# Performance work log

Measured on AMD Instinct MI355X. Metric: run time of the kernel, lower is better.

## Reference

```python
import jax, jax.numpy as jnp
import numpy as np

B, K, T, C, F = 2048, 32, 365, 4, 128  # batch, prototypes, steps, bands, feature_size


def conv1d(x, w, b, pad):
    # x: (B, Cin, T), w: (Cout, Cin, Kw)
    y = jax.lax.conv_general_dilated(x, w, (1,), [(pad, pad)],
                                     dimension_numbers=('NCH', 'OIH', 'NCH'))
    return y + b[None, :, None]


def bn_relu(x, gamma, beta):
    # training-mode BatchNorm1d over (batch, time) per channel
    mu = x.mean((0, 2), keepdims=True)
    var = x.var((0, 2), keepdims=True)
    xn = (x - mu) * jax.lax.rsqrt(var + 1e-5)
    return jax.nn.relu(xn * gamma[None, :, None] + beta[None, :, None])


def encoder(x, w1, b1, g1, be1, w2, b2, g2, be2, w3, b3, g3, be3, fc_w, fc_b):
    # FCNBaseline: 3 conv blocks + global average pool + linear
    h = x.transpose(0, 2, 1)                    # (B, C, T)
    h = bn_relu(conv1d(h, w1, b1, 4), g1, be1)  # (B, 128, T+1)
    h = bn_relu(conv1d(h, w2, b2, 2), g2, be2)  # (B, 256, *)
    h = bn_relu(conv1d(h, w3, b3, 1), g3, be3)  # (B, 128, *)
    return h.mean(-1) @ fc_w.T + fc_b           # (B, F)


def setup_inputs() -> dict:
    key = jax.random.key(0)
    ks = jax.random.split(key, 12)
    input_seq = jax.random.normal(ks[0], (B, T, C), jnp.float32)
    label = jax.random.randint(ks[1], (B,), 0, 9)
    mask = (jax.random.uniform(ks[2], (B, T)) > 0.2).astype(jnp.float32)
    prototypes = jax.random.normal(ks[3], (K, T, C), jnp.float32)
    w1 = jax.random.normal(ks[4], (128, C, 8)) * 0.05
    b1 = jnp.zeros((128,)); g1 = jnp.ones((128,)); be1 = jnp.zeros((128,))
    w2 = jax.random.normal(ks[5], (256, 128, 5)) * 0.05
    b2 = jnp.zeros((256,)); g2 = jnp.ones((256,)); be2 = jnp.zeros((256,))
    w3 = jax.random.normal(ks[6], (128, 256, 3)) * 0.05
    b3 = jnp.zeros((128,)); g3 = jnp.ones((128,)); be3 = jnp.zeros((128,))
    fc_w = jax.random.normal(ks[7], (F, 128)) * 0.05
    fc_b = jnp.zeros((F,))
    off_w = jax.random.normal(ks[8], (K * C, F)) * 0.05
    off_b = jnp.zeros((K * C,))
    return dict(input_seq=input_seq, label=label, mask=mask, prototypes=prototypes,
                w1=w1, b1=b1, g1=g1, be1=be1, w2=w2, b2=b2, g2=g2, be2=be2,
                w3=w3, b3=b3, g3=g3, be3=be3, fc_w=fc_w, fc_b=fc_b,
                off_w=off_w, off_b=off_b)


def reference(input_seq, label, mask, prototypes, w1, b1, g1, be1, w2, b2, g2, be2,
              w3, b3, g3, be3, fc_w, fc_b, off_w, off_b):
    # trans_activ=False (TPS warp disabled), offset_activ=True, unsupervised path
    feat = encoder(input_seq, w1, b1, g1, be1, w2, b2, g2, be2, w3, b3, g3, be3, fc_w, fc_b)
    offset = jnp.tanh(feat @ off_w.T + off_b).reshape(-1, K, 1, C)  # (B,K,1,C)
    protos = prototypes[None] + offset                              # (B,K,T,C)
    diff = input_seq[:, None] - protos                              # (B,K,T,C)
    # masked squared-distance reduce: mask (B,T) broadcasts over (K,C)
    distances = jnp.einsum('bktc,bt->bk', diff * diff, mask)        # (B,K)
    indices = jnp.argmin(distances, axis=1)                         # (B,)
    output_seq = jnp.take_along_axis(protos, indices[:, None, None, None], axis=1)[:, 0]
    return output_seq
```

## Files before the change

### kernel.cpp

```cpp
#include <hip/hip_runtime.h>
#include <hip/hip_bf16.h>

#define BB 2048
#define TIN 365
#define TO 366
#define C1 128
#define C2 256
#define C3 128
#define FF 128

typedef __attribute__((ext_vector_type(4))) float f32x4v;
typedef __attribute__((ext_vector_type(8))) short bf16x8;

__device__ inline unsigned short f2bf(float v) {
  unsigned u = __float_as_uint(v);
  unsigned r = (u + 0x7FFF + ((u >> 16) & 1)) >> 16;
  return (unsigned short)r;
}
__device__ inline float bf2f(unsigned short b) {
  return __uint_as_float(((unsigned)b) << 16);
}

__global__ void wtrans_kernel(const float* __restrict__ wsrc, float* __restrict__ wdst,
                              int Cout, int Cin, int Kw) {
  int n = Cout * Cin * Kw;
  for (int idx = blockIdx.x * 256 + threadIdx.x; idx < n; idx += gridDim.x * 256) {
    int o = idx % Cout;
    int rest = idx / Cout;
    int k = rest % Kw;
    int i = rest / Kw;
    wdst[idx] = wsrc[(o * Cin + i) * Kw + k];
  }
}

__global__ void wprep2_kernel(const float* __restrict__ w2,
                              short* __restrict__ wh, short* __restrict__ wl) {
  int n = 256 * 128 * 5;
  for (int idx = blockIdx.x * 256 + threadIdx.x; idx < n; idx += gridDim.x * 256) {
    int k = idx % 5;
    int rest = idx / 5;
    int i = rest % 128;
    int o = rest / 128;
    float v = w2[idx];
    unsigned short hb = f2bf(v);
    unsigned short lb = f2bf(v - bf2f(hb));
    size_t dst = ((((size_t)k * 4 + (i >> 5)) * 16 + (o >> 4)) * 64 +
                  ((i >> 3) & 3) * 16 + (o & 15)) * 8 + (i & 7);
    wh[dst] = (short)hb;
    wl[dst] = (short)lb;
  }
}
__global__ void wprep3_kernel(const float* __restrict__ w3,
                              short* __restrict__ wh, short* __restrict__ wl) {
  int n = 128 * 256 * 3;
  for (int idx = blockIdx.x * 256 + threadIdx.x; idx < n; idx += gridDim.x * 256) {
    int k = idx % 3;
    int rest = idx / 3;
    int i = rest % 256;
    int o = rest / 256;
    float v = w3[idx];
    unsigned short hb = f2bf(v);
    unsigned short lb = f2bf(v - bf2f(hb));
    size_t dst = ((((size_t)k * 8 + (i >> 5)) * 8 + (o >> 4)) * 64 +
                  ((i >> 3) & 3) * 16 + (o & 15)) * 8 + (i & 7);
    wh[dst] = (short)hb;
    wl[dst] = (short)lb;
  }
}

__global__ void bnparam_kernel(const double* __restrict__ sums,
                               const float* __restrict__ gamma,
                               const float* __restrict__ beta, int Cch,
                               float* __restrict__ scale, float* __restrict__ shift) {
  int i = threadIdx.x;
  if (i < Cch) {
    const double N = (double)BB * (double)TO;
    double mean = sums[i] / N;
    double var = sums[Cch + i] / N - mean * mean;
    double sc = (double)gamma[i] / sqrt(var + 1e-5);
    scale[i] = (float)sc;
    shift[i] = (float)((double)beta[i] - mean * sc);
  }
}

__global__ __launch_bounds__(256) void conv1_stats_kernel(
    const float* __restrict__ x, const float* __restrict__ w1,
    const float* __restrict__ b1, double* __restrict__ sums) {
  __shared__ float4 xs[374];
  __shared__ float ws1[4096];
  int tid = threadIdx.x;
  for (int i = tid; i < 4096; i += 256) ws1[i] = w1[i];
  __syncthreads();
  const int o = tid >> 1, half = tid & 1;
  float wr[32];
#pragma unroll
  for (int i = 0; i < 32; ++i) wr[i] = ws1[o * 32 + i];
  const float bo = b1[o];
  float s1 = 0.f, s2 = 0.f;
  for (int b = blockIdx.x * 8; b < blockIdx.x * 8 + 8; ++b) {
    __syncthreads();
    for (int u = tid; u < 374; u += 256) {
      int t_in = u - 4;
      float4 v = make_float4(0.f, 0.f, 0.f, 0.f);
      if (t_in >= 0 && t_in < TIN) v = *(const float4*)(x + ((size_t)b * TIN + t_in) * 4);
      xs[u] = v;
    }
    __syncthreads();
    for (int t = half * 183; t < half * 183 + 183; ++t) {
      float acc = bo;
#pragma unroll
      for (int k = 0; k < 8; ++k) {
        float4 xv = xs[t + k];
        acc = fmaf(wr[k], xv.x, acc);
        acc = fmaf(wr[8 + k], xv.y, acc);
        acc = fmaf(wr[16 + k], xv.z, acc);
        acc = fmaf(wr[24 + k], xv.w, acc);
      }
      s1 += acc; s2 += acc * acc;
    }
  }
  s1 += __shfl_xor(s1, 1);
  s2 += __shfl_xor(s2, 1);
  if (half == 0) {
    atomicAdd(&sums[o], (double)s1);
    atomicAdd(&sums[C1 + o], (double)s2);
  }
}

template <bool STORE>
__global__ __launch_bounds__(256) void conv2_mfma_kernel(
    const float* __restrict__ x, const float* __restrict__ w1g,
    const float* __restrict__ b1, const float* __restrict__ scale1,
    const float* __restrict__ shift1, const short* __restrict__ w2ph,
    const short* __restrict__ w2pl, const float* __restrict__ b2,
    float* __restrict__ p2, float* __restrict__ h2g) {
  __shared__ float ws1[4096];
  __shared__ float4 xwin[76];
  __shared__ __align__(16) short h1h[68 * 72];
  __shared__ __align__(16) short h1l[68 * 72];
  __shared__ float sstat[512];
  const int tid = threadIdx.x;
  const int tt = blockIdx.x, b = blockIdx.y;
  const int tbase = tt * 64;
  const int slice = (b * 6 + tt) & 63;
  const int w = tid >> 6, lane = tid & 63;
  const int q = lane >> 4, l15 = lane & 15;

  for (int i = tid; i < 4096; i += 256) ws1[i] = w1g[i];
  for (int u = tid; u < 76; u += 256) {
    int tx = tbase - 6 + u;
    float4 v = make_float4(0.f, 0.f, 0.f, 0.f);
    if (tx >= 0 && tx < TIN) v = *(const float4*)(x + ((size_t)b * TIN + tx) * 4);
    xwin[u] = v;
  }
  float b2r[4][4];
#pragma unroll
  for (int om = 0; om < 4; ++om)
#pragma unroll
    for (int r = 0; r < 4; ++r) b2r[om][r] = b2[64 * w + om * 16 + q * 4 + r];

  f32x4v acc[4][4];
#pragma unroll
  for (int om = 0; om < 4; ++om)
#pragma unroll
    for (int nt = 0; nt < 4; ++nt) acc[om][nt] = (f32x4v){0.f, 0.f, 0.f, 0.f};

  const int chl = tid >> 2, qt = tid & 3;
  for (int ic2 = 0; ic2 < 2; ++ic2) {
    __syncthreads();
    {
      int ch = ic2 * 64 + chl;
      float sc = scale1[ch], sh = shift1[ch], bo = b1[ch];
      const float* wr = &ws1[ch * 32];
      for (int j = 0; j < 17; ++j) {
        int u = qt * 17 + j;
        int t = tbase - 2 + u;
        float a = bo;
#pragma unroll
        for (int kk = 0; kk < 8; ++kk) {
          float4 xv = xwin[u + kk];
          a = fmaf(wr[kk], xv.x, a);
          a = fmaf(wr[8 + kk], xv.y, a);
          a = fmaf(wr[16 + kk], xv.z, a);
          a = fmaf(wr[24 + kk], xv.w, a);
        }
        float v = (t >= 0 && t < TO) ? fmaxf(fmaf(sc, a, sh), 0.f) : 0.f;
        unsigned short hb = f2bf(v);
        h1h[u * 72 + chl] = (short)hb;
        h1l[u * 72 + chl] = (short)f2bf(v - bf2f(hb));
      }
    }
    __syncthreads();
    for (int k = 0; k < 5; ++k) {
      for (int ic = 0; ic < 2; ++ic) {
        int icg = ic2 * 2 + ic;
        bf16x8 ah[4], al[4];
#pragma unroll
        for (int om = 0; om < 4; ++om) {
          int og = 4 * w + om;
          size_t base = ((((size_t)k * 4 + icg) * 16 + og) * 64 + lane) * 8;
          ah[om] = *(const bf16x8*)(w2ph + base);
          al[om] = *(const bf16x8*)(w2pl + base);
        }
        int ioff = ic * 32 + q * 8;
#pragma unroll
        for (int nt = 0; nt < 4; ++nt) {
          int u = nt * 16 + l15 + k;
          bf16x8 bh = *(const bf16x8*)&h1h[u * 72 + ioff];
          bf16x8 bl = *(const bf16x8*)&h1l[u * 72 + ioff];
#pragma unroll
          for (int om = 0; om < 4; ++om) {
            acc[om][nt] = __builtin_amdgcn_mfma_f32_16x16x32_bf16(ah[om], bh, acc[om][nt], 0, 0, 0);
            acc[om][nt] = __builtin_amdgcn_mfma_f32_16x16x32_bf16(ah[om], bl, acc[om][nt], 0, 0, 0);
            acc[om][nt] = __builtin_amdgcn_mfma_f32_16x16x32_bf16(al[om], bh, acc[om][nt], 0, 0, 0);
          }
        }
      }
    }
  }
  float ts1[16], ts2[16];
#pragma unroll
  for (int i = 0; i < 16; ++i) { ts1[i] = 0.f; ts2[i] = 0.f; }
#pragma unroll
  for (int om = 0; om < 4; ++om)
#pragma unroll
    for (int nt = 0; nt < 4; ++nt) {
      int t = tbase + nt * 16 + l15;
      if (t < TO) {
#pragma unroll
        for (int r = 0; r < 4; ++r) {
          float v = acc[om][nt][r] + b2r[om][r];
          ts1[om * 4 + r] += v;
          ts2[om * 4 + r] += v * v;
          if (STORE) {
            int o = 64 * w + om * 16 + q * 4 + r;
            h2g[((size_t)b * 256 + o) * 368 + t] = v;
          }
        }
      }
    }
#pragma unroll
  for (int i = 0; i < 16; ++i) {
#pragma unroll
    for (int d = 1; d < 16; d <<= 1) {
      ts1[i] += __shfl_xor(ts1[i], d);
      ts2[i] += __shfl_xor(ts2[i], d);
    }
  }
  if (l15 == 0) {
#pragma unroll
    for (int om = 0; om < 4; ++om)
#pragma unroll
      for (int r = 0; r < 4; ++r) {
        int o = 64 * w + om * 16 + q * 4 + r;
        sstat[o] = ts1[om * 4 + r];
        sstat[256 + o] = ts2[om * 4 + r];
      }
  }
  __syncthreads();
  atomicAdd(&p2[(size_t)tid * 64 + slice], sstat[tid]);
  atomicAdd(&p2[((size_t)tid + 256) * 64 + slice], sstat[tid + 256]);
}

template <int EPI>
__global__ __launch_bounds__(256) void conv3_pass_kernel(
    const float* __restrict__ h2g, const float* __restrict__ scale2,
    const float* __restrict__ shift2, const short* __restrict__ w3ph,
    const short* __restrict__ w3pl, const float* __restrict__ b3,
    const float* __restrict__ scale3, const float* __restrict__ shift3,
    float* __restrict__ p3, float* __restrict__ pooled) {
  __shared__ __align__(16) short h2sh[66 * 264];
  __shared__ __align__(16) short h2sl[66 * 264];
  __shared__ float sstat[256];
  const int tid = threadIdx.x;
  const int tt = blockIdx.x, b = blockIdx.y;
  const int tbase = tt * 64;
  const int slice = (b * 6 + tt) & 63;
  const int w = tid >> 6, lane = tid & 63;
  const int q = lane >> 4, l15 = lane & 15;

  float b3r[2][4], sc3r[2][4], sh3r[2][4];
#pragma unroll
  for (int om = 0; om < 2; ++om)
#pragma unroll
    for (int r = 0; r < 4; ++r) {
      int o = 32 * w + om * 16 + q * 4 + r;
      b3r[om][r] = b3[o];
      if (EPI == 1) { sc3r[om][r] = scale3[o]; sh3r[om][r] = shift3[o]; }
    }

  for (int cc = 0; cc < 64; ++cc) {
    int ch = w * 64 + cc;
    float sc = scale2[ch], sh = shift2[ch];
    const float* src = h2g + ((size_t)b * 256 + ch) * 368;
    int t2 = tbase - 1 + lane;
    float v = 0.f;
    if (t2 >= 0 && t2 < TO) v = fmaxf(fmaf(sc, src[t2], sh), 0.f);
    unsigned short hb = f2bf(v);
    h2sh[lane * 264 + ch] = (short)hb;
    h2sl[lane * 264 + ch] = (short)f2bf(v - bf2f(hb));
    if (lane < 2) {
      int u2 = 64 + lane;
      int t2b = tbase - 1 + u2;
      float vb = 0.f;
      if (t2b >= 0 && t2b < TO) vb = fmaxf(fmaf(sc, src[t2b], sh), 0.f);
      unsigned short hbb = f2bf(vb);
      h2sh[u2 * 264 + ch] = (short)hbb;
      h2sl[u2 * 264 + ch] = (short)f2bf(vb - bf2f(hbb));
    }
  }
  __syncthreads();
  f32x4v acc3[2][4];
#pragma unroll
  for (int om = 0; om < 2; ++om)
#pragma unroll
    for (int nt = 0; nt < 4; ++nt) acc3[om][nt] = (f32x4v){0.f, 0.f, 0.f, 0.f};
  for (int k = 0; k < 3; ++k) {
    for (int icg = 0; icg < 8; ++icg) {
      bf16x8 a3h[2], a3l[2];
#pragma unroll
      for (int om = 0; om < 2; ++om) {
        int og = 2 * w + om;
        size_t base = ((((size_t)k * 8 + icg) * 8 + og) * 64 + lane) * 8;
        a3h[om] = *(const bf16x8*)(w3ph + base);
        a3l[om] = *(const bf16x8*)(w3pl + base);
      }
      int ioff = icg * 32 + q * 8;
#pragma unroll
      for (int nt = 0; nt < 4; ++nt) {
        int u = nt * 16 + l15 + k;
        bf16x8 bh = *(const bf16x8*)&h2sh[u * 264 + ioff];
        bf16x8 bl = *(const bf16x8*)&h2sl[u * 264 + ioff];
#pragma unroll
        for (int om = 0; om < 2; ++om) {
          acc3[om][nt] = __builtin_amdgcn_mfma_f32_16x16x32_bf16(a3h[om], bh, acc3[om][nt], 0, 0, 0);
          acc3[om][nt] = __builtin_amdgcn_mfma_f32_16x16x32_bf16(a3l[om], bh, acc3[om][nt], 0, 0, 0);
          acc3[om][nt] = __builtin_amdgcn_mfma_f32_16x16x32_bf16(a3h[om], bl, acc3[om][nt], 0, 0, 0);
        }
      }
    }
  }
  if (EPI == 0) {
    float ts1[8], ts2[8];
#pragma unroll
    for (int i = 0; i < 8; ++i) { ts1[i] = 0.f; ts2[i] = 0.f; }
#pragma unroll
    for (int om = 0; om < 2; ++om)
#pragma unroll
      for (int nt = 0; nt < 4; ++nt) {
        int t = tbase + nt * 16 + l15;
        if (t < TO) {
#pragma unroll
          for (int r = 0; r < 4; ++r) {
            float v = acc3[om][nt][r] + b3r[om][r];
            ts1[om * 4 + r] += v;
            ts2[om * 4 + r] += v * v;
          }
        }
      }
#pragma unroll
    for (int i = 0; i < 8; ++i) {
#pragma unroll
      for (int d = 1; d < 16; d <<= 1) {
        ts1[i] += __shfl_xor(ts1[i], d);
        ts2[i] += __shfl_xor(ts2[i], d);
      }
    }
    if (l15 == 0) {
#pragma unroll
      for (int om = 0; om < 2; ++om)
#pragma unroll
        for (int r = 0; r < 4; ++r) {
          int o = 32 * w + om * 16 + q * 4 + r;
          sstat[o] = ts1[om * 4 + r];
          sstat[128 + o] = ts2[om * 4 + r];
        }
    }
    __syncthreads();
    atomicAdd(&p3[(size_t)tid * 64 + slice], sstat[tid]);
  } else {
    float ps[8];
#pragma unroll
    for (int i = 0; i < 8; ++i) ps[i] = 0.f;
#pragma unroll
    for (int om = 0; om < 2; ++om)
#pragma unroll
      for (int nt = 0; nt < 4; ++nt) {
        int t = tbase + nt * 16 + l15;
        if (t < TO) {
#pragma unroll
          for (int r = 0; r < 4; ++r) {
            float v = acc3[om][nt][r] + b3r[om][r];
            ps[om * 4 + r] += fmaxf(fmaf(sc3r[om][r], v, sh3r[om][r]), 0.f);
          }
        }
      }
#pragma unroll
    for (int i = 0; i < 8; ++i) {
#pragma unroll
      for (int d = 1; d < 16; d <<= 1) ps[i] += __shfl_xor(ps[i], d);
    }
    if (l15 == 0) {
#pragma unroll
      for (int om = 0; om < 2; ++om)
#pragma unroll
        for (int r = 0; r < 4; ++r) {
          int o = 32 * w + om * 16 + q * 4 + r;
          atomicAdd(&pooled[(size_t)b * 128 + o], ps[om * 4 + r]);
        }
    }
  }
}

template <int EPI>
__global__ __launch_bounds__(256) void fused23_kernel(
    const float* __restrict__ x, const float* __restrict__ w1g,
    const float* __restrict__ b1, const float* __restrict__ scale1,
    const float* __restrict__ shift1, const short* __restrict__ w2ph,
    const short* __restrict__ w2pl, const float* __restrict__ b2,
    const float* __restrict__ scale2, const float* __restrict__ shift2,
    const short* __restrict__ w3ph, const short* __restrict__ w3pl,
    const float* __restrict__ b3, const float* __restrict__ scale3,
    const float* __restrict__ shift3, float* __restrict__ p3,
    float* __restrict__ pooled) {
  __shared__ float4 xwin[80];
  __shared__ __align__(16) short un[34848];
  __shared__ float bn2s[768];
  __shared__ float sstat[256];
  short* h1h = un;
  short* h1l = un + 70 * 72;
  short* h2sh = un;
  short* h2sl = un + 66 * 264;
  const int tid = threadIdx.x;
  const int tt = blockIdx.x, b = blockIdx.y;
  const int tbase = tt * 64;
  const int slice = (b * 6 + tt) & 63;
  const int w = tid >> 6, lane = tid & 63;
  const int q = lane >> 4, l15 = lane & 15;

  for (int u = tid; u < 77; u += 256) {
    int tx = tbase - 7 + u;
    float4 v = make_float4(0.f, 0.f, 0.f, 0.f);
    if (tx >= 0 && tx < TIN) v = *(const float4*)(x + ((size_t)b * TIN + tx) * 4);
    xwin[u] = v;
  }
  bn2s[tid] = b2[tid];
  bn2s[256 + tid] = scale2[tid];
  bn2s[512 + tid] = shift2[tid];

  float b3r[2][4], sc3r[2][4], sh3r[2][4];
#pragma unroll
  for (int om = 0; om < 2; ++om)
#pragma unroll
    for (int r = 0; r < 4; ++r) {
      int o = 32 * w + om * 16 + q * 4 + r;
      b3r[om][r] = b3[o];
      if (EPI == 1) { sc3r[om][r] = scale3[o]; sh3r[om][r] = shift3[o]; }
    }

  f32x4v acc2[4][5];
#pragma unroll
  for (int om = 0; om < 4; ++om)
#pragma unroll
    for (int nt = 0; nt < 5; ++nt) acc2[om][nt] = (f32x4v){0.f, 0.f, 0.f, 0.f};

  const int chl = tid >> 2, qt = tid & 3;
  for (int ic2 = 0; ic2 < 2; ++ic2) {
    int ch = ic2 * 64 + chl;
    float wr[32];
#pragma unroll
    for (int i = 0; i < 32; ++i) wr[i] = w1g[ch * 32 + i];
    float sc = scale1[ch], sh = shift1[ch], bo = b1[ch];
    __syncthreads();
    for (int j = 0; j < 18; ++j) {
      int u1 = qt * 18 + j;
      if (u1 < 70) {
        int t1 = tbase - 3 + u1;
        float a = bo;
#pragma unroll
        for (int kk = 0; kk < 8; ++kk) {
          float4 xv = xwin[u1 + kk];
          a = fmaf(wr[kk], xv.x, a);
          a = fmaf(wr[8 + kk], xv.y, a);
          a = fmaf(wr[16 + kk], xv.z, a);
          a = fmaf(wr[24 + kk], xv.w, a);
        }
        float v = (t1 >= 0 && t1 < TO) ? fmaxf(fmaf(sc, a, sh), 0.f) : 0.f;
        unsigned short hb = f2bf(v);
        h1h[u1 * 72 + chl] = (short)hb;
        h1l[u1 * 72 + chl] = (short)f2bf(v - bf2f(hb));
      }
    }
    __syncthreads();
    for (int k = 0; k < 5; ++k) {
      for (int ic = 0; ic < 2; ++ic) {
        int icg = ic2 * 2 + ic;
        bf16x8 ah[4], al[4];
#pragma unroll
        for (int om = 0; om < 4; ++om) {
          int og = 4 * w + om;
          size_t base = ((((size_t)k * 4 + icg) * 16 + og) * 64 + lane) * 8;
          ah[om] = *(const bf16x8*)(w2ph + base);
          al[om] = *(const bf16x8*)(w2pl + base);
        }
        int ioff = ic * 32 + q * 8;
#pragma unroll
        for (int nt = 0; nt < 5; ++nt) {
          int u1 = nt * 16 + l15 + k;
          if (u1 > 69) u1 = 69;
          bf16x8 bh = *(const bf16x8*)&h1h[u1 * 72 + ioff];
          bf16x8 bl = *(const bf16x8*)&h1l[u1 * 72 + ioff];
#pragma unroll
          for (int om = 0; om < 4; ++om) {
            acc2[om][nt] = __builtin_amdgcn_mfma_f32_16x16x32_bf16(ah[om], bh, acc2[om][nt], 0, 0, 0);
            acc2[om][nt] = __builtin_amdgcn_mfma_f32_16x16x32_bf16(ah[om], bl, acc2[om][nt], 0, 0, 0);
            acc2[om][nt] = __builtin_amdgcn_mfma_f32_16x16x32_bf16(al[om], bh, acc2[om][nt], 0, 0, 0);
          }
        }
      }
    }
  }
  __syncthreads();
#pragma unroll
  for (int om = 0; om < 4; ++om) {
    int og = 4 * w + om;
#pragma unroll
    for (int nt = 0; nt < 5; ++nt) {
      int u2 = nt * 16 + l15;
      if (u2 < 66) {
        int t2 = tbase - 1 + u2;
        bool valid = (t2 >= 0 && t2 < TO);
#pragma unroll
        for (int rp = 0; rp < 2; ++rp) {
          int o = og * 16 + q * 4 + rp * 2;
          float v0 = 0.f, v1 = 0.f;
          if (valid) {
            v0 = fmaxf(fmaf(bn2s[256 + o], acc2[om][nt][rp * 2] + bn2s[o], bn2s[512 + o]), 0.f);
            v1 = fmaxf(fmaf(bn2s[256 + o + 1], acc2[om][nt][rp * 2 + 1] + bn2s[o + 1], bn2s[512 + o + 1]), 0.f);
          }
          unsigned short hb0 = f2bf(v0), hb1 = f2bf(v1);
          *(unsigned*)&h2sh[u2 * 264 + o] = (unsigned)hb0 | ((unsigned)hb1 << 16);
          *(unsigned*)&h2sl[u2 * 264 + o] =
              (unsigned)f2bf(v0 - bf2f(hb0)) | ((unsigned)f2bf(v1 - bf2f(hb1)) << 16);
        }
      }
    }
  }
  __syncthreads();
  f32x4v acc3[2][4];
#pragma unroll
  for (int om = 0; om < 2; ++om)
#pragma unroll
    for (int nt = 0; nt < 4; ++nt) acc3[om][nt] = (f32x4v){0.f, 0.f, 0.f, 0.f};
  for (int k = 0; k < 3; ++k) {
    for (int icg = 0; icg < 8; ++icg) {
      bf16x8 a3h[2], a3l[2];
#pragma unroll
      for (int om = 0; om < 2; ++om) {
        int og = 2 * w + om;
        size_t base = ((((size_t)k * 8 + icg) * 8 + og) * 64 + lane) * 8;
        a3h[om] = *(const bf16x8*)(w3ph + base);
        a3l[om] = *(const bf16x8*)(w3pl + base);
      }
      int ioff = icg * 32 + q * 8;
#pragma unroll
      for (int nt = 0; nt < 4; ++nt) {
        int u = nt * 16 + l15 + k;
        bf16x8 bh = *(const bf16x8*)&h2sh[u * 264 + ioff];
        bf16x8 bl = *(const bf16x8*)&h2sl[u * 264 + ioff];
#pragma unroll
        for (int om = 0; om < 2; ++om) {
          acc3[om][nt] = __builtin_amdgcn_mfma_f32_16x16x32_bf16(a3h[om], bh, acc3[om][nt], 0, 0, 0);
          acc3[om][nt] = __builtin_amdgcn_mfma_f32_16x16x32_bf16(a3l[om], bh, acc3[om][nt], 0, 0, 0);
          acc3[om][nt] = __builtin_amdgcn_mfma_f32_16x16x32_bf16(a3h[om], bl, acc3[om][nt], 0, 0, 0);
        }
      }
    }
  }
  if (EPI == 0) {
    float ts1[8], ts2[8];
#pragma unroll
    for (int i = 0; i < 8; ++i) { ts1[i] = 0.f; ts2[i] = 0.f; }
#pragma unroll
    for (int om = 0; om < 2; ++om)
#pragma unroll
      for (int nt = 0; nt < 4; ++nt) {
        int t = tbase + nt * 16 + l15;
        if (t < TO) {
#pragma unroll
          for (int r = 0; r < 4; ++r) {
            float v = acc3[om][nt][r] + b3r[om][r];
            ts1[om * 4 + r] += v;
            ts2[om * 4 + r] += v * v;
          }
        }
      }
#pragma unroll
    for (int i = 0; i < 8; ++i) {
#pragma unroll
      for (int d = 1; d < 16; d <<= 1) {
        ts1[i] += __shfl_xor(ts1[i], d);
        ts2[i] += __shfl_xor(ts2[i], d);
      }
    }
    if (l15 == 0) {
#pragma unroll
      for (int om = 0; om < 2; ++om)
#pragma unroll
        for (int r = 0; r < 4; ++r) {
          int o = 32 * w + om * 16 + q * 4 + r;
          sstat[o] = ts1[om * 4 + r];
          sstat[128 + o] = ts2[om * 4 + r];
        }
    }
    __syncthreads();
    atomicAdd(&p3[(size_t)tid * 64 + slice], sstat[tid]);
  } else {
    float ps[8];
#pragma unroll
    for (int i = 0; i < 8; ++i) ps[i] = 0.f;
#pragma unroll
    for (int om = 0; om < 2; ++om)
#pragma unroll
      for (int nt = 0; nt < 4; ++nt) {
        int t = tbase + nt * 16 + l15;
        if (t < TO) {
#pragma unroll
          for (int r = 0; r < 4; ++r) {
            float v = acc3[om][nt][r] + b3r[om][r];
            ps[om * 4 + r] += fmaxf(fmaf(sc3r[om][r], v, sh3r[om][r]), 0.f);
          }
        }
      }
#pragma unroll
    for (int i = 0; i < 8; ++i) {
#pragma unroll
      for (int d = 1; d < 16; d <<= 1) ps[i] += __shfl_xor(ps[i], d);
    }
    if (l15 == 0) {
#pragma unroll
      for (int om = 0; om < 2; ++om)
#pragma unroll
        for (int r = 0; r < 4; ++r) {
          int o = 32 * w + om * 16 + q * 4 + r;
          atomicAdd(&pooled[(size_t)b * 128 + o], ps[om * 4 + r]);
        }
    }
  }
}

__global__ __launch_bounds__(64) void reduce_slices_kernel(
    const float* __restrict__ p, double* __restrict__ sums) {
  int c = blockIdx.x, tid = threadIdx.x;
  double s = (double)p[(size_t)c * 64 + tid];
  for (int d = 32; d > 0; d >>= 1) s += __shfl_down(s, d);
  if (tid == 0) sums[c] = s;
}

__global__ __launch_bounds__(128) void head2_kernel(
    const float* __restrict__ pooled, const float* __restrict__ fc_w,
    const float* __restrict__ fc_b, const float* __restrict__ off_w,
    const float* __restrict__ off_b, float* __restrict__ offs) {
  int b = blockIdx.x, tid = threadIdx.x;
  __shared__ float pl[128], feat[128];
  pl[tid] = pooled[(size_t)b * C3 + tid] * (1.0f / 366.0f);
  __syncthreads();
  {
    const float* wr = fc_w + tid * FF;
    float a = fc_b[tid];
    for (int i = 0; i < 128; ++i) a = fmaf(pl[i], wr[i], a);
    feat[tid] = a;
  }
  __syncthreads();
  {
    const float* wr = off_w + tid * FF;
    float z = off_b[tid];
    for (int i = 0; i < 128; ++i) z = fmaf(feat[i], wr[i], z);
    offs[(size_t)b * 128 + tid] = tanhf(z);
  }
}

__global__ __launch_bounds__(256) void dist_kernel(
    const float* __restrict__ x, const float* __restrict__ mask,
    const float* __restrict__ protos, const float* __restrict__ offs,
    float* __restrict__ out) {
  int b = blockIdx.x, tid = threadIdx.x;
  __shared__ float ofl[128];
  __shared__ double dred[256];
  __shared__ int ksel;
  if (tid < 128) ofl[tid] = offs[(size_t)b * 128 + tid];
  __syncthreads();
  int k = tid & 31, tg = tid >> 5;
  float o0 = ofl[k * 4 + 0], o1 = ofl[k * 4 + 1], o2 = ofl[k * 4 + 2], o3 = ofl[k * 4 + 3];
  double acc = 0.0;
  for (int t = tg; t < TIN; t += 8) {
    float4 xv = *(const float4*)(x + ((size_t)b * TIN + t) * 4);
    float4 pv = *(const float4*)(protos + ((size_t)k * TIN + t) * 4);
    float m = mask[(size_t)b * TIN + t];
    float d0 = xv.x - pv.x - o0;
    float d1 = xv.y - pv.y - o1;
    float d2 = xv.z - pv.z - o2;
    float d3 = xv.w - pv.w - o3;
    acc += (double)(m * (d0 * d0 + d1 * d1 + d2 * d2 + d3 * d3));
  }
  dred[tid] = acc;
  __syncthreads();
  if (tid < 32) {
    double s = 0.0;
    for (int g = 0; g < 8; ++g) s += dred[g * 32 + tid];
    dred[tid] = s;
  }
  __syncthreads();
  if (tid == 0) {
    double best = dred[0]; int bi = 0;
    for (int kk = 1; kk < 32; ++kk)
      if (dred[kk] < best) { best = dred[kk]; bi = kk; }
    ksel = bi;
  }
  __syncthreads();
  int km = ksel;
  const float* psrc = protos + (size_t)km * TIN * 4;
  float* dst = out + (size_t)b * TIN * 4;
  for (int u = tid; u < TIN * 4; u += 256)
    dst[u] = psrc[u] + ofl[km * 4 + (u & 3)];
}

extern "C" void kernel_launch(void* const* d_in, const int* in_sizes, int n_in,
                              void* d_out, int out_size, void* d_ws, size_t ws_size,
                              hipStream_t stream) {
  const float* x      = (const float*)d_in[0];
  const float* mask   = (const float*)d_in[2];
  const float* protos = (const float*)d_in[3];
  const float* w1 = (const float*)d_in[4];
  const float* b1 = (const float*)d_in[5];
  const float* g1 = (const float*)d_in[6];
  const float* be1 = (const float*)d_in[7];
  const float* w2 = (const float*)d_in[8];
  const float* b2 = (const float*)d_in[9];
  const float* g2 = (const float*)d_in[10];
  const float* be2 = (const float*)d_in[11];
  const float* w3 = (const float*)d_in[12];
  const float* b3 = (const float*)d_in[13];
  const float* g3 = (const float*)d_in[14];
  const float* be3 = (const float*)d_in[15];
  const float* fc_w = (const float*)d_in[16];
  const float* fc_b = (const float*)d_in[17];
  const float* off_w = (const float*)d_in[18];
  const float* off_b = (const float*)d_in[19];
  float* out = (float*)d_out;
  (void)in_sizes; (void)n_in; (void)out_size;

  char* wsp = (char*)d_ws;
  size_t off = 0;
  auto alloc = [&](size_t bytes) { void* p = wsp + off; off += (bytes + 255) & ~(size_t)255; return p; };
  float* bnp   = (float*)alloc(1024 * 4);
  float* offs  = (float*)alloc((size_t)BB * 128 * 4);
  size_t zero_beg = off;
  double* sums  = (double*)alloc(1024 * 8);
  float* pooled = (float*)alloc((size_t)BB * C3 * 4);
  float* p2     = (float*)alloc((size_t)512 * 64 * 4);
  float* p3     = (float*)alloc((size_t)256 * 64 * 4);
  size_t zero_end = off;
  short* w2ph = (short*)alloc((size_t)256 * 128 * 5 * 2);
  short* w2pl = (short*)alloc((size_t)256 * 128 * 5 * 2);
  short* w3ph = (short*)alloc((size_t)128 * 256 * 3 * 2);
  short* w3pl = (short*)alloc((size_t)128 * 256 * 3 * 2);
  size_t small_end = off;
  const bool mfma_ok = ws_size >= small_end;
  const size_t h2_bytes = (size_t)BB * 256 * 368 * 4;
  float* h2 = (float*)(wsp + small_end);
  const bool h2_ok = ws_size >= small_end + h2_bytes;

  double* sums1 = sums;
  double* sums2 = sums + 256;
  double* sums3 = sums + 768;
  float* scale1 = bnp;        float* shift1 = bnp + 128;
  float* scale2 = bnp + 256;  float* shift2 = bnp + 512;
  float* scale3 = bnp + 768;  float* shift3 = bnp + 896;

  hipMemsetAsync(wsp + zero_beg, 0, zero_end - zero_beg, stream);

  conv1_stats_kernel<<<256, 256, 0, stream>>>(x, w1, b1, sums1);
  bnparam_kernel<<<1, 256, 0, stream>>>(sums1, g1, be1, C1, scale1, shift1);

  if (mfma_ok) {
    wprep2_kernel<<<256, 256, 0, stream>>>(w2, w2ph, w2pl);
    wprep3_kernel<<<128, 256, 0, stream>>>(w3, w3ph, w3pl);

    if (h2_ok) {
      conv2_mfma_kernel<true><<<dim3(6, BB), 256, 0, stream>>>(
          x, w1, b1, scale1, shift1, w2ph, w2pl, b2, p2, h2);
      reduce_slices_kernel<<<512, 64, 0, stream>>>(p2, sums2);
      bnparam_kernel<<<1, 256, 0, stream>>>(sums2, g2, be2, C2, scale2, shift2);
      conv3_pass_kernel<0><<<dim3(6, BB), 256, 0, stream>>>(
          h2, scale2, shift2, w3ph, w3pl, b3, scale3, shift3, p3, pooled);
      reduce_slices_kernel<<<256, 64, 0, stream>>>(p3, sums3);
      bnparam_kernel<<<1, 256, 0, stream>>>(sums3, g3, be3, C3, scale3, shift3);
      conv3_pass_kernel<1><<<dim3(6, BB), 256, 0, stream>>>(
          h2, scale2, shift2, w3ph, w3pl, b3, scale3, shift3, p3, pooled);
    } else {
      conv2_mfma_kernel<false><<<dim3(6, BB), 256, 0, stream>>>(
          x, w1, b1, scale1, shift1, w2ph, w2pl, b2, p2, h2);
      reduce_slices_kernel<<<512, 64, 0, stream>>>(p2, sums2);
      bnparam_kernel<<<1, 256, 0, stream>>>(sums2, g2, be2, C2, scale2, shift2);
      fused23_kernel<0><<<dim3(6, BB), 256, 0, stream>>>(
          x, w1, b1, scale1, shift1, w2ph, w2pl, b2, scale2, shift2,
          w3ph, w3pl, b3, scale3, shift3, p3, pooled);
      reduce_slices_kernel<<<256, 64, 0, stream>>>(p3, sums3);
      bnparam_kernel<<<1, 256, 0, stream>>>(sums3, g3, be3, C3, scale3, shift3);
      fused23_kernel<1><<<dim3(6, BB), 256, 0, stream>>>(
          x, w1, b1, scale1, shift1, w2ph, w2pl, b2, scale2, shift2,
          w3ph, w3pl, b3, scale3, shift3, p3, pooled);
    }
  }

  head2_kernel<<<BB, 128, 0, stream>>>(pooled, fc_w, fc_b, off_w, off_b, offs);
  dist_kernel<<<BB, 256, 0, stream>>>(x, mask, protos, offs, out);
}
```

Measured before the change: 3.914 ms.

## Materialize conv3 output instead of conv2, replacing second conv3 pass with pooling kernel

Before, the path with a large workspace stored the full conv2 output (256 channels) and ran the conv3 MFMA pass twice, once for BN3 statistics and once for the pooled epilogue. Now conv2 only computes statistics. A fused conv1-conv2-conv3 kernel recomputes conv2 and writes the pre-BN conv3 output (128 channels), and a light gap3 kernel applies BN3+ReLU and average-pools it. This halves the intermediate written to and read from memory and removes one full conv3 pass. In exchange, conv2 is recomputed inside the fused kernel.

```diff
diff --git a/kernel.cpp b/kernel.cpp
--- a/kernel.cpp
+++ b/kernel.cpp
@@ -19,18 +19,6 @@
 }
 __device__ inline float bf2f(unsigned short b) {
   return __uint_as_float(((unsigned)b) << 16);
-}
-
-__global__ void wtrans_kernel(const float* __restrict__ wsrc, float* __restrict__ wdst,
-                              int Cout, int Cin, int Kw) {
-  int n = Cout * Cin * Kw;
-  for (int idx = blockIdx.x * 256 + threadIdx.x; idx < n; idx += gridDim.x * 256) {
-    int o = idx % Cout;
-    int rest = idx / Cout;
-    int k = rest % Kw;
-    int i = rest / Kw;
-    wdst[idx] = wsrc[(o * Cin + i) * Kw + k];
-  }
 }
 
 __global__ void wprep2_kernel(const float* __restrict__ w2,
@@ -127,13 +115,12 @@
   }
 }
 
-template <bool STORE>
 __global__ __launch_bounds__(256) void conv2_mfma_kernel(
     const float* __restrict__ x, const float* __restrict__ w1g,
     const float* __restrict__ b1, const float* __restrict__ scale1,
     const float* __restrict__ shift1, const short* __restrict__ w2ph,
     const short* __restrict__ w2pl, const float* __restrict__ b2,
-    float* __restrict__ p2, float* __restrict__ h2g) {
+    float* __restrict__ p2) {
   __shared__ float ws1[4096];
   __shared__ float4 xwin[76];
   __shared__ __align__(16) short h1h[68 * 72];
@@ -232,10 +219,6 @@
           float v = acc[om][nt][r] + b2r[om][r];
           ts1[om * 4 + r] += v;
           ts2[om * 4 + r] += v * v;
-          if (STORE) {
-            int o = 64 * w + om * 16 + q * 4 + r;
-            h2g[((size_t)b * 256 + o) * 368 + t] = v;
-          }
         }
       }
     }
@@ -262,157 +245,7 @@
   atomicAdd(&p2[((size_t)tid + 256) * 64 + slice], sstat[tid + 256]);
 }
 
-template <int EPI>
-__global__ __launch_bounds__(256) void conv3_pass_kernel(
-    const float* __restrict__ h2g, const float* __restrict__ scale2,
-    const float* __restrict__ shift2, const short* __restrict__ w3ph,
-    const short* __restrict__ w3pl, const float* __restrict__ b3,
-    const float* __restrict__ scale3, const float* __restrict__ shift3,
-    float* __restrict__ p3, float* __restrict__ pooled) {
-  __shared__ __align__(16) short h2sh[66 * 264];
-  __shared__ __align__(16) short h2sl[66 * 264];
-  __shared__ float sstat[256];
-  const int tid = threadIdx.x;
-  const int tt = blockIdx.x, b = blockIdx.y;
-  const int tbase = tt * 64;
-  const int slice = (b * 6 + tt) & 63;
-  const int w = tid >> 6, lane = tid & 63;
-  const int q = lane >> 4, l15 = lane & 15;
-
-  float b3r[2][4], sc3r[2][4], sh3r[2][4];
-#pragma unroll
-  for (int om = 0; om < 2; ++om)
-#pragma unroll
-    for (int r = 0; r < 4; ++r) {
-      int o = 32 * w + om * 16 + q * 4 + r;
-      b3r[om][r] = b3[o];
-      if (EPI == 1) { sc3r[om][r] = scale3[o]; sh3r[om][r] = shift3[o]; }
-    }
-
-  for (int cc = 0; cc < 64; ++cc) {
-    int ch = w * 64 + cc;
-    float sc = scale2[ch], sh = shift2[ch];
-    const float* src = h2g + ((size_t)b * 256 + ch) * 368;
-    int t2 = tbase - 1 + lane;
-    float v = 0.f;
-    if (t2 >= 0 && t2 < TO) v = fmaxf(fmaf(sc, src[t2], sh), 0.f);
-    unsigned short hb = f2bf(v);
-    h2sh[lane * 264 + ch] = (short)hb;
-    h2sl[lane * 264 + ch] = (short)f2bf(v - bf2f(hb));
-    if (lane < 2) {
-      int u2 = 64 + lane;
-      int t2b = tbase - 1 + u2;
-      float vb = 0.f;
-      if (t2b >= 0 && t2b < TO) vb = fmaxf(fmaf(sc, src[t2b], sh), 0.f);
-      unsigned short hbb = f2bf(vb);
-      h2sh[u2 * 264 + ch] = (short)hbb;
-      h2sl[u2 * 264 + ch] = (short)f2bf(vb - bf2f(hbb));
-    }
-  }
-  __syncthreads();
-  f32x4v acc3[2][4];
-#pragma unroll
-  for (int om = 0; om < 2; ++om)
-#pragma unroll
-    for (int nt = 0; nt < 4; ++nt) acc3[om][nt] = (f32x4v){0.f, 0.f, 0.f, 0.f};
-  for (int k = 0; k < 3; ++k) {
-    for (int icg = 0; icg < 8; ++icg) {
-      bf16x8 a3h[2], a3l[2];
-#pragma unroll
-      for (int om = 0; om < 2; ++om) {
-        int og = 2 * w + om;
-        size_t base = ((((size_t)k * 8 + icg) * 8 + og) * 64 + lane) * 8;
-        a3h[om] = *(const bf16x8*)(w3ph + base);
-        a3l[om] = *(const bf16x8*)(w3pl + base);
-      }
-      int ioff = icg * 32 + q * 8;
-#pragma unroll
-      for (int nt = 0; nt < 4; ++nt) {
-        int u = nt * 16 + l15 + k;
-        bf16x8 bh = *(const bf16x8*)&h2sh[u * 264 + ioff];
-        bf16x8 bl = *(const bf16x8*)&h2sl[u * 264 + ioff];
-#pragma unroll
-        for (int om = 0; om < 2; ++om) {
-          acc3[om][nt] = __builtin_amdgcn_mfma_f32_16x16x32_bf16(a3h[om], bh, acc3[om][nt], 0, 0, 0);
-          acc3[om][nt] = __builtin_amdgcn_mfma_f32_16x16x32_bf16(a3l[om], bh, acc3[om][nt], 0, 0, 0);
-          acc3[om][nt] = __builtin_amdgcn_mfma_f32_16x16x32_bf16(a3h[om], bl, acc3[om][nt], 0, 0, 0);
-        }
-      }
-    }
-  }
-  if (EPI == 0) {
-    float ts1[8], ts2[8];
-#pragma unroll
-    for (int i = 0; i < 8; ++i) { ts1[i] = 0.f; ts2[i] = 0.f; }
-#pragma unroll
-    for (int om = 0; om < 2; ++om)
-#pragma unroll
-      for (int nt = 0; nt < 4; ++nt) {
-        int t = tbase + nt * 16 + l15;
-        if (t < TO) {
-#pragma unroll
-          for (int r = 0; r < 4; ++r) {
-            float v = acc3[om][nt][r] + b3r[om][r];
-            ts1[om * 4 + r] += v;
-            ts2[om * 4 + r] += v * v;
-          }
-        }
-      }
-#pragma unroll
-    for (int i = 0; i < 8; ++i) {
-#pragma unroll
-      for (int d = 1; d < 16; d <<= 1) {
-        ts1[i] += __shfl_xor(ts1[i], d);
-        ts2[i] += __shfl_xor(ts2[i], d);
-      }
-    }
-    if (l15 == 0) {
-#pragma unroll
-      for (int om = 0; om < 2; ++om)
-#pragma unroll
-        for (int r = 0; r < 4; ++r) {
-          int o = 32 * w + om * 16 + q * 4 + r;
-          sstat[o] = ts1[om * 4 + r];
-          sstat[128 + o] = ts2[om * 4 + r];
-        }
-    }
-    __syncthreads();
-    atomicAdd(&p3[(size_t)tid * 64 + slice], sstat[tid]);
-  } else {
-    float ps[8];
-#pragma unroll
-    for (int i = 0; i < 8; ++i) ps[i] = 0.f;
-#pragma unroll
-    for (int om = 0; om < 2; ++om)
-#pragma unroll
-      for (int nt = 0; nt < 4; ++nt) {
-        int t = tbase + nt * 16 + l15;
-        if (t < TO) {
-#pragma unroll
-          for (int r = 0; r < 4; ++r) {
-            float v = acc3[om][nt][r] + b3r[om][r];
-            ps[om * 4 + r] += fmaxf(fmaf(sc3r[om][r], v, sh3r[om][r]), 0.f);
-          }
-        }
-      }
-#pragma unroll
-    for (int i = 0; i < 8; ++i) {
-#pragma unroll
-      for (int d = 1; d < 16; d <<= 1) ps[i] += __shfl_xor(ps[i], d);
-    }
-    if (l15 == 0) {
-#pragma unroll
-      for (int om = 0; om < 2; ++om)
-#pragma unroll
-        for (int r = 0; r < 4; ++r) {
-          int o = 32 * w + om * 16 + q * 4 + r;
-          atomicAdd(&pooled[(size_t)b * 128 + o], ps[om * 4 + r]);
-        }
-    }
-  }
-}
-
-template <int EPI>
+template <int EPI, bool STOREH3>
 __global__ __launch_bounds__(256) void fused23_kernel(
     const float* __restrict__ x, const float* __restrict__ w1g,
     const float* __restrict__ b1, const float* __restrict__ scale1,
@@ -422,7 +255,7 @@
     const short* __restrict__ w3ph, const short* __restrict__ w3pl,
     const float* __restrict__ b3, const float* __restrict__ scale3,
     const float* __restrict__ shift3, float* __restrict__ p3,
-    float* __restrict__ pooled) {
+    float* __restrict__ pooled, float* __restrict__ h3g) {
   __shared__ float4 xwin[80];
   __shared__ __align__(16) short un[34848];
   __shared__ float bn2s[768];
@@ -592,6 +425,10 @@
             float v = acc3[om][nt][r] + b3r[om][r];
             ts1[om * 4 + r] += v;
             ts2[om * 4 + r] += v * v;
+            if (STOREH3) {
+              int o = 32 * w + om * 16 + q * 4 + r;
+              h3g[((size_t)b * 128 + o) * 368 + t] = v;
+            }
           }
         }
       }
@@ -646,6 +483,24 @@
           atomicAdd(&pooled[(size_t)b * 128 + o], ps[om * 4 + r]);
         }
     }
+  }
+}
+
+__global__ __launch_bounds__(256) void gap3_kernel(
+    const float* __restrict__ h3g, const float* __restrict__ scale3,
+    const float* __restrict__ shift3, float* __restrict__ pooled) {
+  int b = blockIdx.x, tid = threadIdx.x;
+  int w = tid >> 6, lane = tid & 63;
+  for (int cc = 0; cc < 32; ++cc) {
+    int ch = w * 32 + cc;
+    float sc = scale3[ch], sh = shift3[ch];
+    const float* row = h3g + ((size_t)b * 128 + ch) * 368;
+    float s = 0.f;
+    for (int u = lane; u < TO; u += 64)
+      s += fmaxf(fmaf(sc, row[u], sh), 0.f);
+#pragma unroll
+    for (int d = 32; d > 0; d >>= 1) s += __shfl_xor(s, d);
+    if (lane == 0) pooled[(size_t)b * 128 + ch] = s;
   }
 }
 
@@ -766,10 +621,9 @@
   short* w3ph = (short*)alloc((size_t)128 * 256 * 3 * 2);
   short* w3pl = (short*)alloc((size_t)128 * 256 * 3 * 2);
   size_t small_end = off;
-  const bool mfma_ok = ws_size >= small_end;
-  const size_t h2_bytes = (size_t)BB * 256 * 368 * 4;
-  float* h2 = (float*)(wsp + small_end);
-  const bool h2_ok = ws_size >= small_end + h2_bytes;
+  const size_t h3_bytes = (size_t)BB * 128 * 368 * 4;
+  float* h3g = (float*)(wsp + small_end);
+  const bool h3_ok = ws_size >= small_end + h3_bytes;
 
   double* sums1 = sums;
   double* sums2 = sums + 256;
@@ -783,35 +637,30 @@
   conv1_stats_kernel<<<256, 256, 0, stream>>>(x, w1, b1, sums1);
   bnparam_kernel<<<1, 256, 0, stream>>>(sums1, g1, be1, C1, scale1, shift1);
 
-  if (mfma_ok) {
-    wprep2_kernel<<<256, 256, 0, stream>>>(w2, w2ph, w2pl);
-    wprep3_kernel<<<128, 256, 0, stream>>>(w3, w3ph, w3pl);
-
-    if (h2_ok) {
-      conv2_mfma_kernel<true><<<dim3(6, BB), 256, 0, stream>>>(
-          x, w1, b1, scale1, shift1, w2ph, w2pl, b2, p2, h2);
-      reduce_slices_kernel<<<512, 64, 0, stream>>>(p2, sums2);
-      bnparam_kernel<<<1, 256, 0, stream>>>(sums2, g2, be2, C2, scale2, shift2);
-      conv3_pass_kernel<0><<<dim3(6, BB), 256, 0, stream>>>(
-          h2, scale2, shift2, w3ph, w3pl, b3, scale3, shift3, p3, pooled);
-      reduce_slices_kernel<<<256, 64, 0, stream>>>(p3, sums3);
-      bnparam_kernel<<<1, 256, 0, stream>>>(sums3, g3, be3, C3, scale3, shift3);
-      conv3_pass_kernel<1><<<dim3(6, BB), 256, 0, stream>>>(
-          h2, scale2, shift2, w3ph, w3pl, b3, scale3, shift3, p3, pooled);
-    } else {
-      conv2_mfma_kernel<false><<<dim3(6, BB), 256, 0, stream>>>(
-          x, w1, b1, scale1, shift1, w2ph, w2pl, b2, p2, h2);
-      reduce_slices_kernel<<<512, 64, 0, stream>>>(p2, sums2);
-      bnparam_kernel<<<1, 256, 0, stream>>>(sums2, g2, be2, C2, scale2, shift2);
-      fused23_kernel<0><<<dim3(6, BB), 256, 0, stream>>>(
-          x, w1, b1, scale1, shift1, w2ph, w2pl, b2, scale2, shift2,
-          w3ph, w3pl, b3, scale3, shift3, p3, pooled);
-      reduce_slices_kernel<<<256, 64, 0, stream>>>(p3, sums3);
-      bnparam_kernel<<<1, 256, 0, stream>>>(sums3, g3, be3, C3, scale3, shift3);
-      fused23_kernel<1><<<dim3(6, BB), 256, 0, stream>>>(
-          x, w1, b1, scale1, shift1, w2ph, w2pl, b2, scale2, shift2,
-          w3ph, w3pl, b3, scale3, shift3, p3, pooled);
-    }
+  wprep2_kernel<<<256, 256, 0, stream>>>(w2, w2ph, w2pl);
+  wprep3_kernel<<<128, 256, 0, stream>>>(w3, w3ph, w3pl);
+
+  conv2_mfma_kernel<<<dim3(6, BB), 256, 0, stream>>>(
+      x, w1, b1, scale1, shift1, w2ph, w2pl, b2, p2);
+  reduce_slices_kernel<<<512, 64, 0, stream>>>(p2, sums2);
+  bnparam_kernel<<<1, 256, 0, stream>>>(sums2, g2, be2, C2, scale2, shift2);
+
+  if (h3_ok) {
+    fused23_kernel<0, true><<<dim3(6, BB), 256, 0, stream>>>(
+        x, w1, b1, scale1, shift1, w2ph, w2pl, b2, scale2, shift2,
+        w3ph, w3pl, b3, scale3, shift3, p3, pooled, h3g);
+    reduce_slices_kernel<<<256, 64, 0, stream>>>(p3, sums3);
+    bnparam_kernel<<<1, 256, 0, stream>>>(sums3, g3, be3, C3, scale3, shift3);
+    gap3_kernel<<<BB, 256, 0, stream>>>(h3g, scale3, shift3, pooled);
+  } else {
+    fused23_kernel<0, false><<<dim3(6, BB), 256, 0, stream>>>(
+        x, w1, b1, scale1, shift1, w2ph, w2pl, b2, scale2, shift2,
+        w3ph, w3pl, b3, scale3, shift3, p3, pooled, h3g);
+    reduce_slices_kernel<<<256, 64, 0, stream>>>(p3, sums3);
+    bnparam_kernel<<<1, 256, 0, stream>>>(sums3, g3, be3, C3, scale3, shift3);
+    fused23_kernel<1, false><<<dim3(6, BB), 256, 0, stream>>>(
+        x, w1, b1, scale1, shift1, w2ph, w2pl, b2, scale2, shift2,
+        w3ph, w3pl, b3, scale3, shift3, p3, pooled, h3g);
   }
 
   head2_kernel<<<BB, 128, 0, stream>>>(pooled, fc_w, fc_b, off_w, off_b, offs);
```

Measured after the change: 3.873 ms. No clear change (-1.0%).
